# Performance work log

Hardware: AMD Instinct MI355X
Metric: run time of the kernel (lower is better)

Reference implementation:

```python
import jax, jax.numpy as jnp
import numpy as np

NUM_CLASSES = 80
INPUT_HW = (416.0, 416.0)
CONF_THRES = 0.1
NMS_THRES = 0.5
TOPK = 300
ANCHORS = jnp.array([[10.,14.],[23.,27.],[37.,58.],[81.,82.],[135.,169.],[344.,319.]], dtype=jnp.float32)
MASK1 = jnp.array([3,4,5])  # 13x13 head (stride 32)
MASK2 = jnp.array([0,1,2])  # 26x26 head (stride 16)


def _conv(x, w, b, stride):
    y = jax.lax.conv_general_dilated(x, w, (stride, stride), 'SAME',
                                     dimension_numbers=('NCHW', 'OIHW', 'NCHW'))
    return y + b[None, :, None, None]


def _lrelu(x):
    return jnp.where(x > 0, x, 0.1 * x)


def _decode(feat, anchors, C, input_hw):
    # feat: [B, na*(5+C), H, W]
    B, _, H, W = feat.shape
    na = anchors.shape[0]
    p = feat.reshape(B, na, 5 + C, H, W).transpose(0, 1, 3, 4, 2)  # [B,na,H,W,5+C]
    gx = jnp.arange(W, dtype=feat.dtype)
    gy = jnp.arange(H, dtype=feat.dtype)
    x = (jax.nn.sigmoid(p[..., 0]) + gx[None, None, None, :]) / W
    y = (jax.nn.sigmoid(p[..., 1]) + gy[None, None, :, None]) / H
    w = jnp.exp(p[..., 2]) * anchors[None, :, None, None, 0] / input_hw[1]
    h = jnp.exp(p[..., 3]) * anchors[None, :, None, None, 1] / input_hw[0]
    conf = jax.nn.sigmoid(p[..., 4])
    cls = jax.nn.sigmoid(p[..., 5:])
    out = jnp.concatenate([jnp.stack([x, y, w, h, conf], axis=-1), cls], axis=-1)
    return out.reshape(B, na * H * W, 5 + C)


def _correct_boxes(box_xy, box_wh):
    # normalized cx,cy,w,h -> pixel y1,x1,y2,x2 (letterbox correction; identity scale here)
    in_s = jnp.array(INPUT_HW, dtype=jnp.float32)
    img_s = in_s
    yx = box_xy[:, ::-1]
    hw = box_wh[:, ::-1]
    new = jnp.round(img_s * jnp.min(in_s / img_s))
    offset = (in_s - new) / 2.0 / in_s
    scale = in_s / new
    yx = (yx - offset) * scale
    hw = hw * scale
    mins = yx - hw / 2.0
    maxes = yx + hw / 2.0
    return jnp.concatenate([mins, maxes], axis=-1) * jnp.concatenate([img_s, img_s])


def _iou_matrix(b):
    # b: [K,4] as y1,x1,y2,x2
    tl = jnp.maximum(b[:, None, :2], b[None, :, :2])
    br = jnp.minimum(b[:, None, 2:], b[None, :, 2:])
    wh = jnp.clip(br - tl, 0.0)
    inter = wh[..., 0] * wh[..., 1]
    area = (b[:, 2] - b[:, 0]) * (b[:, 3] - b[:, 1])
    return inter / (area[:, None] + area[None, :] - inter + 1e-9)


def _nms_single(pred):
    # pred: [N, 5+C]
    boxes = _correct_boxes(pred[:, 0:2], pred[:, 2:4])  # [N,4]
    obj = pred[:, 4]
    clsp = pred[:, 5:]
    class_conf = jnp.max(clsp, axis=-1)
    label = jnp.argmax(clsp, axis=-1)
    score = obj * class_conf
    score = jnp.where(score >= CONF_THRES, score, 0.0)
    top, idx = jax.lax.top_k(score, TOPK)
    b = boxes[idx]
    lab = label[idx]
    ob = obj[idx]
    cc = class_conf[idx]
    iou = _iou_matrix(b)
    sup = (jax.lax.stop_gradient(iou) > NMS_THRES) & (lab[:, None] == lab[None, :])
    valid = top > 0.0
    ar = jnp.arange(TOPK)

    def body(i, keep):
        is_sup = jnp.any((ar < i) & keep & sup[:, i])
        return keep.at[i].set(keep[i] & jnp.logical_not(is_sup))

    keep = jax.lax.fori_loop(0, TOPK, body, valid)
    out = jnp.concatenate([b, ob[:, None], cc[:, None], lab[:, None].astype(jnp.float32)], axis=-1)
    return jnp.where(keep[:, None], out, 0.0)  # [TOPK, 7]


def _forward(images, w1, b1, w2, b2, w3, b3, w4, b4, w5, b5, wh1, bh1, wh2, bh2):
    x = _lrelu(_conv(images, w1, b1, 2))  # [B,32,208,208]
    x = _lrelu(_conv(x, w2, b2, 2))       # [B,64,104,104]
    x = _lrelu(_conv(x, w3, b3, 2))       # [B,128,52,52]
    x = _lrelu(_conv(x, w4, b4, 2))       # [B,256,26,26]
    feat2 = _conv(x, wh2, bh2, 1)         # [B,255,26,26]
    x = _lrelu(_conv(x, w5, b5, 2))       # [B,512,13,13]
    feat1 = _conv(x, wh1, bh1, 1)         # [B,255,13,13]
    d1 = _decode(feat1, ANCHORS[MASK1], NUM_CLASSES, INPUT_HW)  # [B,507,85]
    d2 = _decode(feat2, ANCHORS[MASK2], NUM_CLASSES, INPUT_HW)  # [B,2028,85]
    pred = jnp.concatenate([d1, d2], axis=1)                    # [B,2535,85]
    return jax.vmap(_nms_single)(pred)                          # [B,300,7]


def setup_inputs() -> dict:
    key = jax.random.key(0)
    ks = jax.random.split(key, 16)
    def w(k, shape, scale=0.05):
        return jax.random.normal(k, shape, dtype=jnp.float32) * scale
    HC = 3 * (5 + NUM_CLASSES)  # 255
    inp = {
        'images': jax.random.normal(ks[0], (8, 3, 416, 416), dtype=jnp.float32),
        'w1': w(ks[1], (32, 3, 3, 3)),   'b1': jnp.zeros((32,), jnp.float32),
        'w2': w(ks[2], (64, 32, 3, 3)),  'b2': jnp.zeros((64,), jnp.float32),
        'w3': w(ks[3], (128, 64, 3, 3)), 'b3': jnp.zeros((128,), jnp.float32),
        'w4': w(ks[4], (256, 128, 3, 3)),'b4': jnp.zeros((256,), jnp.float32),
        'w5': w(ks[5], (512, 256, 3, 3)),'b5': jnp.zeros((512,), jnp.float32),
        'wh1': w(ks[6], (HC, 512, 1, 1), 0.1), 'bh1': jnp.zeros((HC,), jnp.float32),
        'wh2': w(ks[7], (HC, 256, 1, 1), 0.1), 'bh2': jnp.zeros((HC,), jnp.float32),
    }
    return inp


def reference(images, w1, b1, w2, b2, w3, b3, w4, b4, w5, b5, wh1, bh1, wh2, bh2):
    return _forward(images, w1, b1, w2, b2, w3, b3, w4, b4, w5, b5, wh1, bh1, wh2, bh2)
```

## Files before the change

kernel.cpp:

```cpp
#include <hip/hip_runtime.h>
#include <stdint.h>

typedef unsigned long long u64;

__device__ __forceinline__ float sig_(float x) { return 1.0f / (1.0f + expf(-x)); }

#define NCAND 2535
#define NKEEP 300

template <int CIN, int HIN, int WIN, int OCT, int SPLIT, int COUT>
__device__ __forceinline__ void conv_p2_body(
    const float* __restrict__ in, const float* __restrict__ wgt,
    const float* __restrict__ bias, float* __restrict__ out, int bx, int g,
    int bz) {
  constexpr int HOUT = HIN / 2, WOUT = WIN / 2, WP = WOUT / 2;
  constexpr int HWIN = HIN * WIN, HWOUT = HOUT * WOUT;
  constexpr int CS = CIN / SPLIT;
  static_assert(WOUT % 2 == 0 && WIN % 4 == 0, "pair layout");
  const int b = bz / SPLIT, s = bz % SPLIT;
  const int oc0 = g * OCT;
  const int sp = bx * 256 + threadIdx.x;
  if (sp >= HOUT * WP) return;
  const int oy = sp / WP, oxp = sp % WP;
  const int ox0 = oxp * 2;
  const int iy0 = oy * 2, ix0 = oxp * 4;
  const bool okY = (iy0 + 2 < HIN);
  const bool c4v = (ix0 + 4 < WIN);
  const float* inb =
      in + ((size_t)b * CIN + s * CS) * HWIN + (size_t)iy0 * WIN + ix0;
  const float* wbase = wgt + ((size_t)oc0 * CIN + s * CS) * 9;

  float acc0[OCT], acc1[OCT];
#pragma unroll
  for (int u = 0; u < OCT; u++) {
    acc0[u] = 0.0f;
    acc1[u] = 0.0f;
  }

  auto load15 = [&](float v[15], const float* ip) {
#pragma unroll
    for (int ky = 0; ky < 3; ky++) {
      const bool rok = (ky < 2) || okY;
      const float* rp = ip + ky * WIN;
      float4 p = make_float4(0.f, 0.f, 0.f, 0.f);
      float c4 = 0.f;
      if (rok) {
        p = *(const float4*)rp;
        if (c4v) c4 = rp[4];
      }
      v[ky * 5 + 0] = p.x;
      v[ky * 5 + 1] = p.y;
      v[ky * 5 + 2] = p.z;
      v[ky * 5 + 3] = p.w;
      v[ky * 5 + 4] = c4;
    }
  };
  auto fmablk = [&](const float v[15], int ci) {
#pragma unroll
    for (int u = 0; u < OCT; u++) {
#pragma unroll
      for (int ky = 0; ky < 3; ky++) {
#pragma unroll
        for (int kx = 0; kx < 3; kx++) {
          const float w =
              wbase[(size_t)ci * 9 + (size_t)u * CIN * 9 + ky * 3 + kx];
          acc0[u] = fmaf(v[ky * 5 + kx], w, acc0[u]);
          acc1[u] = fmaf(v[ky * 5 + kx + 2], w, acc1[u]);
        }
      }
    }
  };

  float vA[15], vB[15];
  load15(vA, inb);
  if (CS > 1) load15(vB, inb + HWIN);
  for (int ci = 0; ci < CS; ci += 2) {
    float nA[15];
    if (ci + 2 < CS) load15(nA, inb + (size_t)(ci + 2) * HWIN);
    fmablk(vA, ci);
    float nB[15];
    if (ci + 3 < CS) load15(nB, inb + (size_t)(ci + 3) * HWIN);
    if (ci + 1 < CS) fmablk(vB, ci + 1);
    if (ci + 2 < CS) {
#pragma unroll
      for (int k = 0; k < 15; k++) vA[k] = nA[k];
    }
    if (ci + 3 < CS) {
#pragma unroll
      for (int k = 0; k < 15; k++) vB[k] = nB[k];
    }
  }

  const size_t obase =
      (SPLIT == 1 ? (size_t)b * COUT : (size_t)(s * 8 + b) * COUT);
  float* ob = out + (obase + oc0) * HWOUT + (size_t)oy * WOUT + ox0;
  if (SPLIT == 1) {
#pragma unroll
    for (int u = 0; u < OCT; u++) {
      float r0 = acc0[u] + bias[oc0 + u];
      float r1 = acc1[u] + bias[oc0 + u];
      r0 = r0 > 0.0f ? r0 : 0.1f * r0;
      r1 = r1 > 0.0f ? r1 : 0.1f * r1;
      *(float2*)(ob + (size_t)u * HWOUT) = make_float2(r0, r1);
    }
  } else {
#pragma unroll
    for (int u = 0; u < OCT; u++)
      *(float2*)(ob + (size_t)u * HWOUT) = make_float2(acc0[u], acc1[u]);
  }
}

__global__ __launch_bounds__(256) void k_conv1(const float* __restrict__ i,
                                               const float* __restrict__ w,
                                               const float* __restrict__ b,
                                               float* __restrict__ o) {
  const int fb = blockIdx.x;
  const int bz = fb & 7;
  const int r = fb >> 3;
  conv_p2_body<3, 416, 416, 8, 1, 32>(i, w, b, o, r % 85, r / 85, bz);
}
__global__ __launch_bounds__(256) void k_conv2(const float* __restrict__ i,
                                               const float* __restrict__ w,
                                               const float* __restrict__ b,
                                               float* __restrict__ o) {
  const int fb = blockIdx.x;
  const int bz = fb & 7;
  const int r = fb >> 3;
  conv_p2_body<32, 208, 208, 8, 1, 64>(i, w, b, o, r % 22, r / 22, bz);
}

__global__ __launch_bounds__(256) void k_conv3_repack(
    const float* __restrict__ i, const float* __restrict__ w,
    float* __restrict__ o, const float* __restrict__ w4,
    float* __restrict__ w4r) {
  const int fb = blockIdx.x;
  if (fb < 1536) {
    const int low3 = fb & 7;
    int r = fb >> 3;
    const int x = r % 6;
    r /= 6;
    const int zhi = r & 1;
    const int g = r >> 1;
    conv_p2_body<64, 104, 104, 8, 2, 128>(i, w, nullptr, o, x, g,
                                          low3 + 8 * zhi);
    return;
  }
  const int base = (fb - 1536) * 256 + threadIdx.x;
  for (int gid = base; gid < 294912; gid += 160 * 256) {
    const int oc = gid / (128 * 9), r = gid % (128 * 9);
    const int ci = r / 9, k = r % 9;
    const int g = oc / 8, u = oc % 8, s = ci / 32, cl = ci % 32;
    w4r[(size_t)(g * 4 + s) * 2304 + (cl * 8 + u) * 9 + k] = w4[gid];
  }
}

__global__ __launch_bounds__(256) void k_reduce_pad3(
    const float* __restrict__ P3, const float* __restrict__ bias,
    float* __restrict__ x3p) {
  const int gid = blockIdx.x * 256 + threadIdx.x;
  if (gid >= 8 * 128 * 3024) return;
  const int c = gid / 3024;
  const int r = gid % 3024;
  const int y = r / 56, x = r % 56;
  float a = 0.0f;
  if (y < 52 && x < 52) {
    const int src = c * 2704 + y * 52 + x;
    a = P3[src] + P3[2768896 + src];
    a += bias[c & 127];
    a = a > 0.0f ? a : 0.1f * a;
  }
  x3p[gid] = a;
}

__device__ __forceinline__ void conv4z2_body(const float* __restrict__ in,
                                             const float* __restrict__ wgt,
                                             float* __restrict__ out, int g,
                                             int s, int bp, int x) {
  constexpr int OCT = 8, CS = 32;
  constexpr int PHW = 3024, PW = 56;
  constexpr int HWOUT = 676, WOUT = 26, COUT = 256;
  const int b0 = bp * 2;
  const int sp = x * 256 + threadIdx.x;
  if (sp >= HWOUT) return;
  const int oy = sp / WOUT, ox = sp % WOUT;
  const float* inb0 =
      in + ((size_t)b0 * 128 + s * CS) * PHW + (size_t)(oy * 2) * PW + ox * 2;
  const float* inb1 = inb0 + (size_t)128 * PHW;
  const float* wb = wgt + (size_t)(g * 4 + s) * (CS * OCT * 9);

  float acc0[OCT], acc1[OCT];
#pragma unroll
  for (int u = 0; u < OCT; u++) {
    acc0[u] = 0.0f;
    acc1[u] = 0.0f;
  }

  auto load9 = [&](float v[9], const float* ip) {
#pragma unroll
    for (int ky = 0; ky < 3; ky++) {
      const float2 p = *(const float2*)(ip + ky * PW);
      v[ky * 3 + 0] = p.x;
      v[ky * 3 + 1] = p.y;
      v[ky * 3 + 2] = ip[ky * PW + 2];
    }
  };
  auto fmablk2 = [&](const float v0[9], const float v1[9], int ci) {
#pragma unroll
    for (int u = 0; u < OCT; u++) {
#pragma unroll
      for (int k = 0; k < 9; k++) {
        const float w = wb[(size_t)(ci * OCT + u) * 9 + k];
        acc0[u] = fmaf(v0[k], w, acc0[u]);
        acc1[u] = fmaf(v1[k], w, acc1[u]);
      }
    }
  };

  float vA0[9], vA1[9], vB0[9], vB1[9];
  load9(vA0, inb0);
  load9(vA1, inb1);
#pragma unroll 1
  for (int ci = 0; ci < CS; ci += 2) {
    load9(vB0, inb0 + (size_t)(ci + 1) * PHW);
    load9(vB1, inb1 + (size_t)(ci + 1) * PHW);
    fmablk2(vA0, vA1, ci);
    load9(vA0, inb0 + (size_t)(ci + 2) * PHW);
    load9(vA1, inb1 + (size_t)(ci + 2) * PHW);
    fmablk2(vB0, vB1, ci + 1);
  }

  float* ob0 = out + ((size_t)(s * 8 + b0) * COUT + g * OCT) * HWOUT + sp;
  float* ob1 = ob0 + (size_t)COUT * HWOUT;
#pragma unroll
  for (int u = 0; u < OCT; u++) {
    ob0[(size_t)u * HWOUT] = acc0[u];
    ob1[(size_t)u * HWOUT] = acc1[u];
  }
}

__global__ __launch_bounds__(256) void k_conv4_repack(
    const float* __restrict__ x3p, const float* __restrict__ w4r,
    float* __restrict__ P, const float* __restrict__ w5,
    const float* __restrict__ wh2, const float* __restrict__ wh1,
    float* __restrict__ w5r, float* __restrict__ wh2r,
    float* __restrict__ wh1r) {
  const int fb = blockIdx.x;
  if (fb < 1536) {
    const int low4 = fb & 15;
    const int bp = low4 >> 2, s = low4 & 3;
    const int r = fb >> 4;
    const int x = r % 3, g = r / 3;
    conv4z2_body(x3p, w4r, P, g, s, bp, x);
    return;
  }
  const int base = (fb - 1536) * 256 + threadIdx.x;
  for (int gid = base; gid < 1375488; gid += 1024 * 256) {
    if (gid < 1179648) {
      const int oc = gid / (256 * 9), r = gid % (256 * 9);
      const int ci = r / 9, k = r % 9;
      const int g = oc / 8, u = oc % 8, s = ci / 32, cl = ci % 32;
      w5r[(((size_t)(g * 8 + s) * 32 + cl) * 8 + u) * 9 + k] = w5[gid];
    } else if (gid < 1179648 + 65280) {
      const int t = gid - 1179648;
      const int oc = t / 256, ci = t % 256;
      const int g = oc / 17, u = oc % 17, s = ci / 128, cl = ci % 128;
      wh2r[((size_t)(g * 2 + s) * 128 + cl) * 17 + u] = wh2[t];
    } else {
      const int t = gid - 1179648 - 65280;
      const int oc = t / 512, ci = t % 512;
      const int g = oc / 17, u = oc % 17, s = ci / 32, cl = ci % 32;
      wh1r[((size_t)(g * 16 + s) * 32 + cl) * 17 + u] = wh1[t];
    }
  }
}

__global__ __launch_bounds__(256) void k_reduce_pad4(
    const float* __restrict__ P, const float* __restrict__ bias,
    float* __restrict__ x4p) {
  const int gid = blockIdx.x * 256 + threadIdx.x;
  if (gid >= 8 * 256 * 756) return;
  const int c = gid / 756;
  const int r = gid % 756;
  const int y = r / 28, x = r % 28;
  float a = 0.0f;
  if (y < 26 && x < 26) {
    const int src = c * 676 + y * 26 + x;
#pragma unroll
    for (int s = 0; s < 4; s++) a += P[(size_t)s * 1384448 + src];
    a += bias[c & 255];
    a = a > 0.0f ? a : 0.1f * a;
  }
  x4p[gid] = a;
}

template <int CIN, int OCT, int SPLIT, bool PAD>
__device__ __forceinline__ void head_body(const float* __restrict__ in,
                                          const float* __restrict__ wgt,
                                          float* __restrict__ out, int HW,
                                          int bx, int g, int bz) {
  constexpr int CS = CIN / SPLIT;
  const int sp = bx * 256 + threadIdx.x;
  if (sp >= HW) return;
  const int oc0 = g * OCT;
  const int b = bz / SPLIT, s = bz % SPLIT;
  const int IHW = PAD ? 756 : HW;
  const int psp = PAD ? (sp / 26) * 28 + (sp % 26) : sp;
  const float* ip = in + ((size_t)b * CIN + s * CS) * IHW + psp;
  const float* wb = wgt + (size_t)(g * SPLIT + s) * CS * OCT;
  float acc[OCT];
#pragma unroll
  for (int u = 0; u < OCT; u++) acc[u] = 0.0f;

  auto fma4 = [&](const float v[4], int base) {
#pragma unroll
    for (int j = 0; j < 4; j++) {
#pragma unroll
      for (int u = 0; u < OCT; u++)
        acc[u] = fmaf(v[j], wb[(size_t)(base + j) * OCT + u], acc[u]);
    }
  };

  float vA[4], vB[4];
#pragma unroll
  for (int j = 0; j < 4; j++) {
    vA[j] = ip[(size_t)j * IHW];
    vB[j] = ip[(size_t)(4 + j) * IHW];
  }
  for (int c0 = 0; c0 < CS; c0 += 8) {
    float nA[4];
    if (c0 + 8 < CS) {
#pragma unroll
      for (int j = 0; j < 4; j++) nA[j] = ip[(size_t)(c0 + 8 + j) * IHW];
    }
    fma4(vA, c0);
    float nB[4];
    if (c0 + 12 < CS) {
#pragma unroll
      for (int j = 0; j < 4; j++) nB[j] = ip[(size_t)(c0 + 12 + j) * IHW];
    }
    fma4(vB, c0 + 4);
    if (c0 + 8 < CS) {
#pragma unroll
      for (int j = 0; j < 4; j++) vA[j] = nA[j];
    }
    if (c0 + 12 < CS) {
#pragma unroll
      for (int j = 0; j < 4; j++) vB[j] = nB[j];
    }
  }
#pragma unroll
  for (int u = 0; u < OCT; u++)
    out[((size_t)(s * 8 + b) * 255 + oc0 + u) * HW + sp] = acc[u];
}

__device__ __forceinline__ void conv5z2_body(const float* __restrict__ in,
                                             const float* __restrict__ wgt,
                                             float* __restrict__ out, int g,
                                             int s, int bp) {
  constexpr int OCT = 8, CS = 32;
  constexpr int PHW = 756, PW = 28;
  constexpr int HWOUT = 169, WOUT = 13, COUT = 512;
  const int b0 = bp * 2;
  const int sp = threadIdx.x;
  if (sp >= HWOUT) return;
  const int oy = sp / WOUT, ox = sp % WOUT;
  const float* inb0 =
      in + ((size_t)b0 * 256 + s * CS) * PHW + (size_t)(oy * 2) * PW + ox * 2;
  const float* inb1 = inb0 + (size_t)256 * PHW;
  const float* wb = wgt + (size_t)(g * 8 + s) * (CS * OCT * 9);

  float acc0[OCT], acc1[OCT];
#pragma unroll
  for (int u = 0; u < OCT; u++) {
    acc0[u] = 0.0f;
    acc1[u] = 0.0f;
  }

  auto load9 = [&](float v[9], const float* ip) {
#pragma unroll
    for (int ky = 0; ky < 3; ky++) {
      const float2 p = *(const float2*)(ip + ky * PW);
      v[ky * 3 + 0] = p.x;
      v[ky * 3 + 1] = p.y;
      v[ky * 3 + 2] = ip[ky * PW + 2];
    }
  };
  auto fmablk2 = [&](const float v0[9], const float v1[9], int ci) {
#pragma unroll
    for (int u = 0; u < OCT; u++) {
#pragma unroll
      for (int k = 0; k < 9; k++) {
        const float w = wb[(size_t)(ci * OCT + u) * 9 + k];
        acc0[u] = fmaf(v0[k], w, acc0[u]);
        acc1[u] = fmaf(v1[k], w, acc1[u]);
      }
    }
  };

  float vA0[9], vA1[9], vB0[9], vB1[9];
  load9(vA0, inb0);
  load9(vA1, inb1);
#pragma unroll 1
  for (int ci = 0; ci < CS; ci += 2) {
    load9(vB0, inb0 + (size_t)(ci + 1) * PHW);
    load9(vB1, inb1 + (size_t)(ci + 1) * PHW);
    fmablk2(vA0, vA1, ci);
    load9(vA0, inb0 + (size_t)(ci + 2) * PHW);
    load9(vA1, inb1 + (size_t)(ci + 2) * PHW);
    fmablk2(vB0, vB1, ci + 1);
  }

  float* ob0 = out + ((size_t)(s * 8 + b0) * COUT + g * OCT) * HWOUT + sp;
  float* ob1 = ob0 + (size_t)COUT * HWOUT;
#pragma unroll
  for (int u = 0; u < OCT; u++) {
    ob0[(size_t)u * HWOUT] = acc0[u];
    ob1[(size_t)u * HWOUT] = acc1[u];
  }
}

__global__ __launch_bounds__(256) void k_h2c5(const float* __restrict__ x4p,
                                              const float* __restrict__ w5r,
                                              const float* __restrict__ wh2r,
                                              float* __restrict__ P5,
                                              float* __restrict__ Ph2) {
  const int fb = blockIdx.x;
  if (fb < 2048) {
    const int s = fb & 7;
    const int r = fb >> 3;
    const int bp = r & 3;
    const int g = r >> 2;
    conv5z2_body(x4p, w5r, P5, g, s, bp);
  } else {
    const int id = fb - 2048;
    const int low3 = id & 7;
    int r = id >> 3;
    const int x = r % 3;
    r /= 3;
    const int zhi = r & 1;
    const int g = r >> 1;
    head_body<256, 17, 2, true>(x4p, wh2r, Ph2, 676, x, g, low3 + 8 * zhi);
  }
}

__global__ __launch_bounds__(256) void k_head1(const float* __restrict__ i,
                                               const float* __restrict__ w,
                                               float* __restrict__ o) {
  head_body<512, 17, 16, false>(i, w, o, 169, blockIdx.x, blockIdx.y,
                                blockIdx.z);
}

template <int SPLIT, bool LRELU>
__device__ __forceinline__ void reduce_body(const float* __restrict__ P,
                                            const float* __restrict__ bias,
                                            float* __restrict__ out, int COUT,
                                            int HWOUT, int N, int gid) {
  if (gid >= N) return;
  float a = 0.0f;
#pragma unroll
  for (int s = 0; s < SPLIT; s++) a += P[(size_t)s * N + gid];
  const int oc = (gid / HWOUT) % COUT;
  a += bias[oc];
  if (LRELU) a = a > 0.0f ? a : 0.1f * a;
  out[gid] = a;
}

template <int SPLIT, bool LRELU>
__global__ __launch_bounds__(256) void reduce_bias(
    const float* __restrict__ P, const float* __restrict__ bias,
    float* __restrict__ out, int COUT, int HWOUT, int N) {
  reduce_body<SPLIT, LRELU>(P, bias, out, COUT, HWOUT, N,
                            blockIdx.x * 256 + threadIdx.x);
}

__global__ __launch_bounds__(256) void k_reduce_h2c5(
    const float* __restrict__ P5, const float* __restrict__ Ph2,
    const float* __restrict__ b5, const float* __restrict__ bh2,
    float* __restrict__ x5, float* __restrict__ f2) {
  const int fb = blockIdx.x;
  if (fb < 2704) {
    reduce_body<8, true>(P5, b5, x5, 512, 169, 692224,
                         fb * 256 + threadIdx.x);
  } else {
    reduce_body<2, false>(Ph2, bh2, f2, 255, 676, 1379040,
                          (fb - 2704) * 256 + threadIdx.x);
  }
}

__global__ __launch_bounds__(256) void decode_kernel(
    const float* __restrict__ feat1, const float* __restrict__ feat2,
    float* __restrict__ cand, u64* __restrict__ keys) {
  const int gid = blockIdx.x * 256 + threadIdx.x;
  if (gid >= 8 * NCAND) return;
  const int b = gid / NCAND;
  const int i = gid % NCAND;
  const float* p;
  int rem, HW, W;
  float aw, ah;
  if (i < 507) {
    const int a = i / 169;
    rem = i % 169;
    HW = 169;
    W = 13;
    const float AW[3] = {81.f, 135.f, 344.f};
    const float AH[3] = {82.f, 169.f, 319.f};
    aw = AW[a];
    ah = AH[a];
    p = feat1 + ((size_t)b * 255 + a * 85) * 169 + rem;
  } else {
    const int j = i - 507;
    const int a = j / 676;
    rem = j % 676;
    HW = 676;
    W = 26;
    const float AW[3] = {10.f, 23.f, 37.f};
    const float AH[3] = {14.f, 27.f, 58.f};
    aw = AW[a];
    ah = AH[a];
    p = feat2 + ((size_t)b * 255 + a * 85) * 676 + rem;
  }
  const int gy = rem / W, gx = rem % W;
  const float invW = 1.0f / (float)W;
  float cx = (sig_(p[0]) + (float)gx) * invW;
  float cy = (sig_(p[(size_t)HW]) + (float)gy) * invW;
  float bw = expf(p[(size_t)2 * HW]) * aw / 416.0f;
  float bh = expf(p[(size_t)3 * HW]) * ah / 416.0f;
  float obj = sig_(p[(size_t)4 * HW]);
  float best = p[(size_t)5 * HW];
  int lab = 0;
  for (int c = 1; c < 80; ++c) {
    float v = p[(size_t)(5 + c) * HW];
    if (v > best) {
      best = v;
      lab = c;
    }
  }
  float cc = sig_(best);
  float score = obj * cc;
  if (score < 0.1f) score = 0.0f;
  float* o = cand + (size_t)gid * 8;
  o[0] = (cy - bh * 0.5f) * 416.0f;
  o[1] = (cx - bw * 0.5f) * 416.0f;
  o[2] = (cy + bh * 0.5f) * 416.0f;
  o[3] = (cx + bw * 0.5f) * 416.0f;
  o[4] = obj;
  o[5] = cc;
  o[6] = (float)lab;
  o[7] = score;
  keys[gid] = ((u64)__float_as_uint(score) << 32) |
              (u64)(0xFFFFFFFFu - (unsigned)i);
}

__global__ __launch_bounds__(256) void rank_select_kernel(
    const u64* __restrict__ keys, int* __restrict__ sel) {
  const int b = blockIdx.y;
  __shared__ u64 k[NCAND];
  const u64* kb = keys + (size_t)b * NCAND;
  for (int t = threadIdx.x; t < NCAND; t += 256) k[t] = kb[t];
  __syncthreads();
  const int idx = blockIdx.x * 256 + threadIdx.x;
  if (idx >= NCAND) return;
  const u64 me = k[idx];
  int rank = 0;
#pragma unroll 4
  for (int j = 0; j < NCAND; j++) rank += (k[j] > me) ? 1 : 0;
  if (rank < NKEEP) sel[b * NKEEP + rank] = idx;
}

__global__ __launch_bounds__(256) void nms_mask_kernel(
    const float* __restrict__ cand, const int* __restrict__ sel,
    u64* __restrict__ mskg) {
  const int b = blockIdx.y;
  const int r0 = blockIdx.x * 30;
  const int tid = threadIdx.x;
  const float* cb = cand + (size_t)b * NCAND * 8;

  __shared__ float4 bxv[NKEEP];
  __shared__ int lv[NKEEP];

  for (int t = tid; t < NKEEP; t += 256) {
    const int idx = sel[b * NKEEP + t];
    const float* c = cb + (size_t)idx * 8;
    const float4 c0 = *(const float4*)c;
    const float4 c1 = *(const float4*)(c + 4);
    bxv[t] = c0;
    lv[t] = (int)c1.z | ((c1.w > 0.0f) ? 0x10000 : 0);
  }
  __syncthreads();

  if (tid >= 150) return;
  const int t = r0 + tid / 5;
  const int q = tid % 5;
  u64 w = 0;
  const int lvt = lv[t];
  if (lvt & 0x10000) {
    const float4 a = bxv[t];
    const float aarea = (a.z - a.x) * (a.w - a.y);
    const int jlo = (q * 64 > t + 1) ? q * 64 : t + 1;
    const int jhi = (q * 64 + 64 < NKEEP) ? q * 64 + 64 : NKEEP;
    for (int j = jlo; j < jhi; ++j) {
      if (lv[j] == lvt) {
        const float4 bbj = bxv[j];
        const float ty = fmaxf(a.x, bbj.x), tx = fmaxf(a.y, bbj.y);
        const float ey = fminf(a.z, bbj.z), ex = fminf(a.w, bbj.w);
        const float dy = fmaxf(ey - ty, 0.0f), dx = fmaxf(ex - tx, 0.0f);
        const float inter = dy * dx;
        const float barea = (bbj.z - bbj.x) * (bbj.w - bbj.y);
        const float iou = inter / (aarea + barea - inter + 1e-9f);
        if (iou > 0.5f) w |= 1ull << (j & 63);
      }
    }
  }
  mskg[((size_t)b * NKEEP + t) * 5 + q] = w;
}

__global__ __launch_bounds__(256) void nms_scan_kernel(
    const float* __restrict__ cand, const int* __restrict__ sel,
    const u64* __restrict__ mskg, float* __restrict__ out) {
  const int b = blockIdx.x;
  const int tid = threadIdx.x;
  const float* cb = cand + (size_t)b * NCAND * 8;

  __shared__ float4 bxv[NKEEP];
  __shared__ float2 oc2[NKEEP];
  __shared__ int lv[NKEEP];
  __shared__ u64 msk[NKEEP][5];
  __shared__ u64 validw[5];
  __shared__ u64 keepw[5];

  for (int t = tid; t < NKEEP; t += 256) {
    const int idx = sel[b * NKEEP + t];
    const float* c = cb + (size_t)idx * 8;
    const float4 c0 = *(const float4*)c;
    const float4 c1 = *(const float4*)(c + 4);
    bxv[t] = c0;
    oc2[t] = make_float2(c1.x, c1.y);
    lv[t] = (int)c1.z | ((c1.w > 0.0f) ? 0x10000 : 0);
  }
  {
    const u64* mb = mskg + (size_t)b * NKEEP * 5;
    u64* md = &msk[0][0];
    for (int t = tid; t < NKEEP * 5; t += 256) md[t] = mb[t];
  }
  __syncthreads();

  {
    const u64 m1 = __ballot((lv[tid] & 0x10000) != 0);
    if ((tid & 63) == 0) validw[tid >> 6] = m1;
    const u64 m2 = __ballot(tid < 44 && (lv[tid + 256] & 0x10000) != 0);
    if (tid == 0) validw[4] = m2;
  }
  __syncthreads();

  u64 kw0 = validw[0], kw1 = validw[1], kw2 = validw[2], kw3 = validw[3],
      kw4 = validw[4];
  auto scanq = [&](u64& kwq, int q, int nb) {
    for (int bit = 0; bit < nb; ++bit) {
      const int r = q * 64 + bit;
      const u64 m = 0ull - ((kwq >> bit) & 1ull);
      kw0 &= ~(msk[r][0] & m);
      kw1 &= ~(msk[r][1] & m);
      kw2 &= ~(msk[r][2] & m);
      kw3 &= ~(msk[r][3] & m);
      kw4 &= ~(msk[r][4] & m);
    }
  };
  scanq(kw0, 0, 64);
  scanq(kw1, 1, 64);
  scanq(kw2, 2, 64);
  scanq(kw3, 3, 64);
  scanq(kw4, 4, NKEEP - 256);

  if (tid == 0) {
    keepw[0] = kw0;
    keepw[1] = kw1;
    keepw[2] = kw2;
    keepw[3] = kw3;
    keepw[4] = kw4;
  }
  __syncthreads();

  float* ob = out + (size_t)b * NKEEP * 7;
  for (int t = tid; t < NKEEP; t += 256) {
    const bool k = (keepw[t >> 6] >> (t & 63)) & 1ull;
    float* r = ob + (size_t)t * 7;
    if (k) {
      const float4 a = bxv[t];
      const float2 o2 = oc2[t];
      r[0] = a.x;
      r[1] = a.y;
      r[2] = a.z;
      r[3] = a.w;
      r[4] = o2.x;
      r[5] = o2.y;
      r[6] = (float)(lv[t] & 0xFFFF);
    } else {
      r[0] = 0.0f; r[1] = 0.0f; r[2] = 0.0f; r[3] = 0.0f;
      r[4] = 0.0f; r[5] = 0.0f; r[6] = 0.0f;
    }
  }
}

extern "C" void kernel_launch(void* const* d_in, const int* in_sizes, int n_in,
                              void* d_out, int out_size, void* d_ws,
                              size_t ws_size, hipStream_t stream) {
  const float* images = (const float*)d_in[0];
  const float* w1 = (const float*)d_in[1];
  const float* b1 = (const float*)d_in[2];
  const float* w2 = (const float*)d_in[3];
  const float* b2 = (const float*)d_in[4];
  const float* w3 = (const float*)d_in[5];
  const float* b3 = (const float*)d_in[6];
  const float* w4 = (const float*)d_in[7];
  const float* b4 = (const float*)d_in[8];
  const float* w5 = (const float*)d_in[9];
  const float* b5 = (const float*)d_in[10];
  const float* wh1 = (const float*)d_in[11];
  const float* bh1 = (const float*)d_in[12];
  const float* wh2 = (const float*)d_in[13];
  const float* bh2 = (const float*)d_in[14];
  float* ws = (float*)d_ws;

  float* x1 = ws + 0;
  float* x2 = ws + 11075584;
  float* P3 = ws + 5537792;
  float* x3p = ws + 0;
  float* w4r = ws + 3200000;
  float* x4p = ws + 0;
  float* f2 = ws + 4153344;
  float* x5 = ws + 5532384;
  float* f1 = ws + 6224608;
  float* cd = ws + 6569368;
  u64* keys = (u64*)(ws + 6731608);
  int* sel = (int*)(ws + 6772168);
  u64* mskg = (u64*)(ws + 6774568);
  float* P = ws + 11075584;
  float* w5r = ws + 6224608;
  float* wh2r = ws + 7404256;
  float* wh1r = ws + 7469536;
  float* Ph2 = ws + 7600096;

  k_conv1<<<2720, 256, 0, stream>>>(images, w1, b1, x1);
  k_conv2<<<1408, 256, 0, stream>>>(x1, w2, b2, x2);
  k_conv3_repack<<<1696, 256, 0, stream>>>(x2, w3, P3, w4, w4r);
  k_reduce_pad3<<<12096, 256, 0, stream>>>(P3, b3, x3p);
  k_conv4_repack<<<2560, 256, 0, stream>>>(x3p, w4r, P, w5, wh2, wh1, w5r, wh2r, wh1r);
  k_reduce_pad4<<<6048, 256, 0, stream>>>(P, b4, x4p);
  k_h2c5<<<2768, 256, 0, stream>>>(x4p, w5r, wh2r, P, Ph2);
  k_reduce_h2c5<<<2704 + 5388, 256, 0, stream>>>(P, Ph2, b5, bh2, x5, f2);
  k_head1<<<dim3(1, 15, 128), 256, 0, stream>>>(x5, wh1r, P);
  reduce_bias<16, false><<<(344760 + 255) / 256, 256, 0, stream>>>(P, bh1, f1, 255, 169, 344760);

  decode_kernel<<<80, 256, 0, stream>>>(f1, f2, cd, keys);
  rank_select_kernel<<<dim3(10, 8), 256, 0, stream>>>(keys, sel);
  nms_mask_kernel<<<dim3(10, 8), 256, 0, stream>>>(cd, sel, mskg);
  nms_scan_kernel<<<8, 256, 0, stream>>>(cd, sel, mskg, (float*)d_out);
}
```

Baseline: 496.7 us.

## Share conv2/conv3 weight loads across two images per thread

Conv2 and conv3 are rewritten so each thread computes one output pixel for two batch images at once, instead of two adjacent pixels for one image. Each weight read then feeds two FMAs, and the next channel's inputs are loaded while the current one computes, so the input loads overlap the math. Grid sizes change to match the new mapping. The cost is more live registers per thread, and the old paired-pixel float2 store layout is lost, which may reduce occupancy.

```diff
diff --git a/kernel.cpp b/kernel.cpp
--- a/kernel.cpp
+++ b/kernel.cpp
@@ -119,33 +119,170 @@
   const int r = fb >> 3;
   conv_p2_body<3, 416, 416, 8, 1, 32>(i, w, b, o, r % 85, r / 85, bz);
 }
-__global__ __launch_bounds__(256) void k_conv2(const float* __restrict__ i,
-                                               const float* __restrict__ w,
-                                               const float* __restrict__ b,
-                                               float* __restrict__ o) {
+
+__global__ __launch_bounds__(256) void k_conv2z2(
+    const float* __restrict__ in, const float* __restrict__ wgt,
+    const float* __restrict__ bias, float* __restrict__ out) {
+  constexpr int OCT = 8, CIN = 32, HIN = 208, WIN = 208;
+  constexpr int HWIN = 43264, HWOUT = 10816, WOUT = 104, COUT = 64;
   const int fb = blockIdx.x;
-  const int bz = fb & 7;
-  const int r = fb >> 3;
-  conv_p2_body<32, 208, 208, 8, 1, 64>(i, w, b, o, r % 22, r / 22, bz);
+  const int bp = fb & 3;
+  const int r = fb >> 2;
+  const int x = r % 43;
+  const int g = r / 43;
+  const int b0 = bp * 2;
+  const int sp = x * 256 + threadIdx.x;
+  if (sp >= HWOUT) return;
+  const int oy = sp / WOUT, ox = sp % WOUT;
+  const int iy0 = oy * 2, ix0 = ox * 2;
+  const bool okY = (iy0 + 2 < HIN);
+  const bool okX = (ix0 + 2 < WIN);
+  const float* inb0 = in + (size_t)b0 * CIN * HWIN + (size_t)iy0 * WIN + ix0;
+  const float* inb1 = inb0 + (size_t)CIN * HWIN;
+  const float* wb = wgt + (size_t)g * OCT * CIN * 9;
+
+  float acc0[OCT], acc1[OCT];
+#pragma unroll
+  for (int u = 0; u < OCT; u++) {
+    acc0[u] = 0.0f;
+    acc1[u] = 0.0f;
+  }
+
+  auto load9 = [&](float v[9], const float* ip) {
+#pragma unroll
+    for (int ky = 0; ky < 3; ky++) {
+      const bool rok = (ky < 2) || okY;
+      float2 p = make_float2(0.f, 0.f);
+      float c2 = 0.f;
+      if (rok) {
+        p = *(const float2*)(ip + ky * WIN);
+        if (okX) c2 = ip[ky * WIN + 2];
+      }
+      v[ky * 3 + 0] = p.x;
+      v[ky * 3 + 1] = p.y;
+      v[ky * 3 + 2] = c2;
+    }
+  };
+  auto fmablk2 = [&](const float v0[9], const float v1[9], int ci) {
+#pragma unroll
+    for (int u = 0; u < OCT; u++) {
+#pragma unroll
+      for (int k = 0; k < 9; k++) {
+        const float w = wb[(size_t)u * (CIN * 9) + ci * 9 + k];
+        acc0[u] = fmaf(v0[k], w, acc0[u]);
+        acc1[u] = fmaf(v1[k], w, acc1[u]);
+      }
+    }
+  };
+
+  float vA0[9], vA1[9], vB0[9], vB1[9];
+  load9(vA0, inb0);
+  load9(vA1, inb1);
+#pragma unroll 1
+  for (int ci = 0; ci < CIN; ci += 2) {
+    load9(vB0, inb0 + (size_t)(ci + 1) * HWIN);
+    load9(vB1, inb1 + (size_t)(ci + 1) * HWIN);
+    fmablk2(vA0, vA1, ci);
+    load9(vA0, inb0 + (size_t)(ci + 2) * HWIN);
+    load9(vA1, inb1 + (size_t)(ci + 2) * HWIN);
+    fmablk2(vB0, vB1, ci + 1);
+  }
+
+  float* ob0 = out + ((size_t)b0 * COUT + g * OCT) * HWOUT + sp;
+  float* ob1 = ob0 + (size_t)COUT * HWOUT;
+#pragma unroll
+  for (int u = 0; u < OCT; u++) {
+    float r0 = acc0[u] + bias[g * OCT + u];
+    float r1 = acc1[u] + bias[g * OCT + u];
+    r0 = r0 > 0.0f ? r0 : 0.1f * r0;
+    r1 = r1 > 0.0f ? r1 : 0.1f * r1;
+    ob0[(size_t)u * HWOUT] = r0;
+    ob1[(size_t)u * HWOUT] = r1;
+  }
 }
 
 __global__ __launch_bounds__(256) void k_conv3_repack(
-    const float* __restrict__ i, const float* __restrict__ w,
-    float* __restrict__ o, const float* __restrict__ w4,
+    const float* __restrict__ in, const float* __restrict__ wgt,
+    float* __restrict__ P3, const float* __restrict__ w4,
     float* __restrict__ w4r) {
   const int fb = blockIdx.x;
-  if (fb < 1536) {
+  if (fb < 1408) {
+    constexpr int OCT = 8, CS = 32, HIN = 104, WIN = 104;
+    constexpr int HWIN = 10816, HWOUT = 2704, WOUT = 52, COUT = 128;
     const int low3 = fb & 7;
-    int r = fb >> 3;
-    const int x = r % 6;
-    r /= 6;
-    const int zhi = r & 1;
-    const int g = r >> 1;
-    conv_p2_body<64, 104, 104, 8, 2, 128>(i, w, nullptr, o, x, g,
-                                          low3 + 8 * zhi);
+    const int s = low3 >> 2, bp = low3 & 3;
+    const int r = fb >> 3;
+    const int x = r % 11, g = r / 11;
+    const int b0 = bp * 2;
+    const int sp = x * 256 + threadIdx.x;
+    if (sp >= HWOUT) return;
+    const int oy = sp / WOUT, ox = sp % WOUT;
+    const int iy0 = oy * 2, ix0 = ox * 2;
+    const bool okY = (iy0 + 2 < HIN);
+    const bool okX = (ix0 + 2 < WIN);
+    const float* inb0 =
+        in + ((size_t)b0 * 64 + s * CS) * HWIN + (size_t)iy0 * WIN + ix0;
+    const float* inb1 = inb0 + (size_t)64 * HWIN;
+    const float* wb = wgt + ((size_t)(g * OCT) * 64 + s * CS) * 9;
+
+    float acc0[OCT], acc1[OCT];
+#pragma unroll
+    for (int u = 0; u < OCT; u++) {
+      acc0[u] = 0.0f;
+      acc1[u] = 0.0f;
+    }
+
+    auto load9 = [&](float v[9], const float* ip) {
+#pragma unroll
+      for (int ky = 0; ky < 3; ky++) {
+        const bool rok = (ky < 2) || okY;
+        float2 p = make_float2(0.f, 0.f);
+        float c2 = 0.f;
+        if (rok) {
+          p = *(const float2*)(ip + ky * WIN);
+          if (okX) c2 = ip[ky * WIN + 2];
+        }
+        v[ky * 3 + 0] = p.x;
+        v[ky * 3 + 1] = p.y;
+        v[ky * 3 + 2] = c2;
+      }
+    };
+    auto fmablk2 = [&](const float v0[9], const float v1[9], int ci) {
+#pragma unroll
+      for (int u = 0; u < OCT; u++) {
+#pragma unroll
+        for (int k = 0; k < 9; k++) {
+          const float w = wb[(size_t)u * (64 * 9) + ci * 9 + k];
+          acc0[u] = fmaf(v0[k], w, acc0[u]);
+          acc1[u] = fmaf(v1[k], w, acc1[u]);
+        }
+      }
+    };
+
+    float vA0[9], vA1[9], vB0[9], vB1[9];
+    load9(vA0, inb0);
+    load9(vA1, inb1);
+#pragma unroll 1
+    for (int ci = 0; ci < CS; ci += 2) {
+      const int cn = (ci + 2) & (CS - 1);
+      load9(vB0, inb0 + (size_t)(ci + 1) * HWIN);
+      load9(vB1, inb1 + (size_t)(ci + 1) * HWIN);
+      fmablk2(vA0, vA1, ci);
+      load9(vA0, inb0 + (size_t)cn * HWIN);
+      load9(vA1, inb1 + (size_t)cn * HWIN);
+      fmablk2(vB0, vB1, ci + 1);
+    }
+
+    float* ob0 = P3 + ((size_t)(s * 8 + b0) * COUT + g * OCT) * HWOUT + sp;
+    float* ob1 = ob0 + (size_t)COUT * HWOUT;
+#pragma unroll
+    for (int u = 0; u < OCT; u++) {
+      ob0[(size_t)u * HWOUT] = acc0[u];
+      ob1[(size_t)u * HWOUT] = acc1[u];
+    }
     return;
   }
-  const int base = (fb - 1536) * 256 + threadIdx.x;
+  const int base = (fb - 1408) * 256 + threadIdx.x;
   for (int gid = base; gid < 294912; gid += 160 * 256) {
     const int oc = gid / (128 * 9), r = gid % (128 * 9);
     const int ci = r / 9, k = r % 9;
@@ -741,8 +878,8 @@
   float* Ph2 = ws + 7600096;
 
   k_conv1<<<2720, 256, 0, stream>>>(images, w1, b1, x1);
-  k_conv2<<<1408, 256, 0, stream>>>(x1, w2, b2, x2);
-  k_conv3_repack<<<1696, 256, 0, stream>>>(x2, w3, P3, w4, w4r);
+  k_conv2z2<<<1376, 256, 0, stream>>>(x1, w2, b2, x2);
+  k_conv3_repack<<<1568, 256, 0, stream>>>(x2, w3, P3, w4, w4r);
   k_reduce_pad3<<<12096, 256, 0, stream>>>(P3, b3, x3p);
   k_conv4_repack<<<2560, 256, 0, stream>>>(x3p, w4r, P, w5, wh2, wh1, w5r, wh2r, wh1r);
   k_reduce_pad4<<<6048, 256, 0, stream>>>(P, b4, x4p);
```

New measurement: 545.6 us. +9.8%, slower.
